# Performance work log

Measured on AMD Instinct MI355X. Metric: run time of the kernel, lower is better.

The kernel has to match this reference:

```python
import jax, jax.numpy as jnp
import numpy as np

B, S, CACHE, HID, NH, NKV, HD, INTER = 2, 1024, 2048, 2048, 8, 1, 256, 16384
EPS = 1e-6
SOFTCAP = 50.0
SCALE = HD ** -0.5  # query_pre_attn_scalar is None -> head_dim**-0.5
NEG = -1e9


def _rms(x, w, eps=EPS):
    # Gemma RMSNorm: fp32 norm, output scaled by (1 + weight)
    x32 = x.astype(jnp.float32)
    n = x32 * jax.lax.rsqrt(jnp.mean(x32 * x32, axis=-1, keepdims=True) + eps)
    return (n * (1.0 + w)).astype(x.dtype)


def _rope(x, cos, sin):
    # half-split complex rotation (Gemma apply_rotary_emb): first half real, second half imag
    d2 = x.shape[-1] // 2
    x1, x2 = x[..., :d2], x[..., d2:]
    c = cos[None, :, None, :]
    s = sin[None, :, None, :]
    return jnp.concatenate([x1 * c - x2 * s, x1 * s + x2 * c], axis=-1).astype(x.dtype)


def setup_inputs() -> dict:
    key = jax.random.key(0)
    ks = jax.random.split(key, 8)
    sc = lambda k, sh, f: jax.random.normal(k, sh, jnp.float32) * f
    inp = {}
    inp["hidden_states"] = sc(ks[0], (B, S, HID), 1.0)
    inv = 1.0 / (10000.0 ** (np.arange(0, HD, 2, dtype=np.float32) / HD))
    t = np.arange(S, dtype=np.float32)[:, None] * inv[None, :]
    inp["cos"] = jnp.asarray(np.cos(t), jnp.float32)
    inp["sin"] = jnp.asarray(np.sin(t), jnp.float32)
    inp["kv_write_indices"] = jnp.arange(S, dtype=jnp.int32)
    inp["k_cache"] = jnp.zeros((B, CACHE, NKV, HD), jnp.float32)
    inp["v_cache"] = jnp.zeros((B, CACHE, NKV, HD), jnp.float32)
    i = jnp.arange(S)[:, None]
    j = jnp.arange(CACHE)[None, :]
    inp["mask"] = jnp.where(j <= i, 0.0, NEG).astype(jnp.float32)[None, None]  # [1,1,S,CACHE]
    inp["w_qkv"] = sc(ks[1], ((NH + 2 * NKV) * HD, HID), 0.02)
    inp["w_o"] = sc(ks[2], (HID, NH * HD), 0.02)
    inp["w_gate"] = sc(ks[3], (INTER, HID), 0.02)
    inp["w_up"] = sc(ks[4], (INTER, HID), 0.02)
    inp["w_down"] = sc(ks[5], (HID, INTER), 0.02)
    inp["ln_in"] = jnp.zeros((HID,), jnp.float32)
    inp["ln_post"] = jnp.zeros((HID,), jnp.float32)
    inp["q_norm"] = jnp.zeros((HD,), jnp.float32)
    inp["k_norm"] = jnp.zeros((HD,), jnp.float32)
    return inp


def reference(hidden_states, cos, sin, kv_write_indices, k_cache, v_cache, mask,
              w_qkv, w_o, w_gate, w_up, w_down, ln_in, ln_post, q_norm, k_norm):
    # ---- attention sub-block ----
    res = hidden_states
    x = _rms(hidden_states, ln_in)
    qkv = x @ w_qkv.T  # [B,S,(NH+2*NKV)*HD]
    xq, xk, xv = jnp.split(qkv, [NH * HD, NH * HD + NKV * HD], axis=-1)
    xq = xq.reshape(B, S, NH, HD)
    xk = xk.reshape(B, S, NKV, HD)
    xv = xv.reshape(B, S, NKV, HD)
    xq = _rms(xq, q_norm)  # QK-norm
    xk = _rms(xk, k_norm)
    xq = _rope(xq, cos, sin)
    xk = _rope(xk, cos, sin)
    # KV-cache write (index_copy_ on dim 1)
    k_cache = k_cache.at[:, kv_write_indices].set(xk)
    v_cache = v_cache.at[:, kv_write_indices].set(xv)
    key = jnp.repeat(k_cache, NH // NKV, axis=2)  # [B,CACHE,NH,HD]
    val = jnp.repeat(v_cache, NH // NKV, axis=2)
    scores = jnp.einsum('bshd,bthd->bhst', xq * SCALE, key)  # [B,NH,S,CACHE]
    scores = jnp.tanh(scores / SOFTCAP) * SOFTCAP            # logit softcapping
    probs = jax.nn.softmax(scores + mask, axis=-1)
    out = jnp.einsum('bhst,bthd->bshd', probs, val).reshape(B, S, NH * HD)
    h = res + out @ w_o.T
    # ---- MLP sub-block ----
    res = h
    x = _rms(h, ln_post)
    gate = jax.nn.gelu(x @ w_gate.T, approximate=True)
    up = x @ w_up.T
    return res + (gate * up) @ w_down.T
```

## Files before the change

### kernel.cpp

```cpp
#include <hip/hip_runtime.h>
#include <hip/hip_bf16.h>

typedef __attribute__((ext_vector_type(8))) short short8;
typedef __attribute__((ext_vector_type(4))) float f32x4;
typedef unsigned short u16;

#define B_N 2
#define S_N 1024
#define HID_N 2048
#define NH_N 8
#define HD_N 256
#define INTER_N 16384

#define GLB(p) ((const __attribute__((address_space(1))) void*)(p))
#define AS3(p) ((__attribute__((address_space(3))) void*)(p))

__device__ inline u16 f2b_rn(float f) {
    union { float f; unsigned int u; } x; x.f = f;
    unsigned int r = x.u + 0x7fffu + ((x.u >> 16) & 1u);
    return (u16)(r >> 16);
}
__device__ inline float b2f(u16 h) {
    union { unsigned int u; float f; } x; x.u = ((unsigned int)h) << 16;
    return x.f;
}
__device__ inline float gelu_tanh(float x) {
    float x3 = x * x * x;
    return 0.5f * x * (1.f + tanhf(0.7978845608028654f * (x + 0.044715f * x3)));
}

__global__ __launch_bounds__(256) void convert_f2b(const float* __restrict__ in,
                                                   u16* __restrict__ out, int n4) {
    int i = blockIdx.x * 256 + threadIdx.x;
    int stride = gridDim.x * 256;
    for (; i < n4; i += stride) {
        float4 v = reinterpret_cast<const float4*>(in)[i];
        u16 o[4] = { f2b_rn(v.x), f2b_rn(v.y), f2b_rn(v.z), f2b_rn(v.w) };
        reinterpret_cast<ulonglong1*>(out)[i] = *reinterpret_cast<ulonglong1*>(o);
    }
}

__global__ __launch_bounds__(256) void rmsnorm_k(const float* __restrict__ x,
                                                 const float* __restrict__ w,
                                                 u16* __restrict__ out) {
    const int row = blockIdx.x;
    const int tid = threadIdx.x;
    const float* xr = x + (size_t)row * HID_N;
    const float4* xr4 = reinterpret_cast<const float4*>(xr);
    float4 a = xr4[tid * 2], b = xr4[tid * 2 + 1];
    float s = a.x*a.x + a.y*a.y + a.z*a.z + a.w*a.w
            + b.x*b.x + b.y*b.y + b.z*b.z + b.w*b.w;
    for (int off = 32; off > 0; off >>= 1) s += __shfl_xor(s, off, 64);
    __shared__ float red[4];
    if ((tid & 63) == 0) red[tid >> 6] = s;
    __syncthreads();
    float tot = red[0] + red[1] + red[2] + red[3];
    float inv = rsqrtf(tot * (1.0f / HID_N) + 1e-6f);
    const float4* w4 = reinterpret_cast<const float4*>(w);
    float4 wa = w4[tid * 2], wb = w4[tid * 2 + 1];
    short8 o;
    o[0] = (short)f2b_rn(a.x * inv * (1.f + wa.x));
    o[1] = (short)f2b_rn(a.y * inv * (1.f + wa.y));
    o[2] = (short)f2b_rn(a.z * inv * (1.f + wa.z));
    o[3] = (short)f2b_rn(a.w * inv * (1.f + wa.w));
    o[4] = (short)f2b_rn(b.x * inv * (1.f + wb.x));
    o[5] = (short)f2b_rn(b.y * inv * (1.f + wb.y));
    o[6] = (short)f2b_rn(b.z * inv * (1.f + wb.z));
    o[7] = (short)f2b_rn(b.w * inv * (1.f + wb.w));
    reinterpret_cast<short8*>(out + (size_t)row * HID_N)[tid] = o;
}

__global__ __launch_bounds__(256) void qkv_post_k(const float* __restrict__ qkv,
                                                  const float* __restrict__ cosb,
                                                  const float* __restrict__ sinb,
                                                  const int* __restrict__ kvw,
                                                  const float* __restrict__ qn,
                                                  const float* __restrict__ kn,
                                                  u16* __restrict__ qb,
                                                  u16* __restrict__ kb,
                                                  u16* __restrict__ vt) {
    const int bs = blockIdx.x;
    const int b = bs >> 10, s = bs & 1023;
    const int tid = threadIdx.x;
    const float* row = qkv + (size_t)bs * 2560;
    __shared__ float buf[256];
    __shared__ float red[4];
    const int sdst = kvw[s];
    const float cv = cosb[s * 128 + (tid & 127)];
    const float sv = sinb[s * 128 + (tid & 127)];
    for (int vi = 0; vi < 9; ++vi) {
        float val = row[vi * 256 + tid];
        float ss = val * val;
        for (int off = 32; off > 0; off >>= 1) ss += __shfl_xor(ss, off, 64);
        __syncthreads();
        if ((tid & 63) == 0) red[tid >> 6] = ss;
        __syncthreads();
        float ms = (red[0] + red[1] + red[2] + red[3]) * (1.f / 256.f) + 1e-6f;
        const float* nw = (vi < 8) ? qn : kn;
        float nrm = val * rsqrtf(ms) * (1.f + nw[tid]);
        buf[tid] = nrm;
        __syncthreads();
        float o;
        if (tid < 128) o = buf[tid] * cv - buf[tid + 128] * sv;
        else           o = buf[tid - 128] * sv + buf[tid] * cv;
        if (vi < 8) {
            qb[(((size_t)(b * 8 + vi)) * 1024 + s) * 256 + tid] = f2b_rn(o * 0.0625f);
        } else {
            kb[((size_t)(b * 1024 + sdst)) * 256 + tid] = f2b_rn(o);
        }
    }
    float vv = row[2304 + tid];
    vt[((size_t)(b * 256 + tid)) * 1024 + sdst] = f2b_rn(vv);
}

__global__ __launch_bounds__(256) void attn_k(const u16* __restrict__ qb,
                                              const u16* __restrict__ kb,
                                              const u16* __restrict__ vt,
                                              float* __restrict__ po,
                                              float* __restrict__ pl) {
    const int qt = blockIdx.x;
    const int h  = blockIdx.y;
    const int c  = blockIdx.z >> 1;
    const int b  = blockIdx.z & 1;
    if (c == 1 && qt < 8) return;
    const int tid = threadIdx.x, lane = tid & 63, wid = tid >> 6;
    const int g = lane >> 4, li = lane & 15;
    const int q0 = qt * 64 + wid * 16;
    const int kv_lo = c * 512;
    __shared__ u16 pbuf[4][16 * 32];

    short8 qf[8];
    const size_t qbase = (((size_t)(b * 8 + h)) * 1024 + q0 + li) * 256;
    #pragma unroll
    for (int kk = 0; kk < 8; ++kk)
        qf[kk] = *reinterpret_cast<const short8*>(qb + qbase + kk * 32 + g * 8);

    f32x4 o[16], o1;
    #pragma unroll
    for (int d = 0; d < 16; ++d) o[d] = f32x4{0.f, 0.f, 0.f, 0.f};
    o1 = f32x4{0.f, 0.f, 0.f, 0.f};
    short8 onesf;
    #pragma unroll
    for (int j = 0; j < 8; ++j) onesf[j] = (short)0x3F80;

    const int nt = (min(kv_lo + 512, q0 + 16) - kv_lo + 31) >> 5;
    const int prd = li * 32 + ((g * 8) ^ (((li >> 2) & 3) * 8));

    for (int t = 0; t < nt; ++t) {
        const int kv0 = kv_lo + t * 32;
        f32x4 sc[2];
        sc[0] = f32x4{0.f, 0.f, 0.f, 0.f};
        sc[1] = f32x4{0.f, 0.f, 0.f, 0.f};
        #pragma unroll
        for (int ch = 0; ch < 2; ++ch) {
            const size_t kbase = ((size_t)(b * 1024 + kv0 + ch * 16 + li)) * 256;
            #pragma unroll
            for (int kk = 0; kk < 8; ++kk) {
                short8 kf = *reinterpret_cast<const short8*>(kb + kbase + kk * 32 + g * 8);
                sc[ch] = __builtin_amdgcn_mfma_f32_16x16x32_bf16(qf[kk], kf, sc[ch], 0, 0, 0);
            }
        }
        #pragma unroll
        for (int reg = 0; reg < 4; ++reg) {
            const int qrow = q0 + g * 4 + reg;
            const int prow = g * 4 + reg;
            const int pswz = ((prow >> 2) & 3) * 8;
            #pragma unroll
            for (int ch = 0; ch < 2; ++ch) {
                const int col = kv0 + ch * 16 + li;
                float s = sc[ch][reg];
                float e = exp2f(s * 0.05770780163555854f);
                float th = 1.f - 2.f * __builtin_amdgcn_rcpf(e + 1.f);
                float pv = exp2f(th * 72.13475204444817f);
                pv = (col <= qrow) ? pv : 0.f;
                pbuf[wid][prow * 32 + ((ch * 16 + li) ^ pswz)] = f2b_rn(pv);
            }
        }
        short8 pf = *reinterpret_cast<const short8*>(&pbuf[wid][prd]);
        o1 = __builtin_amdgcn_mfma_f32_16x16x32_bf16(pf, onesf, o1, 0, 0, 0);
        #pragma unroll
        for (int dth = 0; dth < 2; ++dth) {
            short8 vf[8];
            #pragma unroll
            for (int d8 = 0; d8 < 8; ++d8) {
                const int dt = dth * 8 + d8;
                vf[d8] = *reinterpret_cast<const short8*>(
                    vt + ((size_t)(b * 256 + dt * 16 + li)) * 1024 + kv0 + g * 8);
            }
            #pragma unroll
            for (int d8 = 0; d8 < 8; ++d8)
                o[dth * 8 + d8] = __builtin_amdgcn_mfma_f32_16x16x32_bf16(pf, vf[d8], o[dth * 8 + d8], 0, 0, 0);
        }
    }
    const size_t pbase = ((size_t)((c * 2 + b) * 8 + h)) * 1024;
    #pragma unroll
    for (int reg = 0; reg < 4; ++reg) {
        const int row = q0 + g * 4 + reg;
        #pragma unroll
        for (int dt = 0; dt < 16; ++dt)
            po[(pbase + row) * 256 + dt * 16 + li] = o[dt][reg];
        if (li == 0) pl[pbase + row] = o1[reg];
    }
}

__global__ __launch_bounds__(256) void attn_red_k(const float* __restrict__ po,
                                                  const float* __restrict__ pl,
                                                  u16* __restrict__ out) {
    const int gid = blockIdx.x;
    const int b = gid >> 10, s = gid & 1023;
    const int tid = threadIdx.x;
    const int h = tid >> 5, d0 = (tid & 31) * 8;
    const size_t r0 = ((size_t)(b * 8 + h)) * 1024 + s;
    const size_t r1 = ((size_t)((2 + b) * 8 + h)) * 1024 + s;
    float l = pl[r0];
    float4 a0 = *reinterpret_cast<const float4*>(po + r0 * 256 + d0);
    float4 a1 = *reinterpret_cast<const float4*>(po + r0 * 256 + d0 + 4);
    if (s >= 512) {
        l += pl[r1];
        float4 b0 = *reinterpret_cast<const float4*>(po + r1 * 256 + d0);
        float4 b1 = *reinterpret_cast<const float4*>(po + r1 * 256 + d0 + 4);
        a0.x += b0.x; a0.y += b0.y; a0.z += b0.z; a0.w += b0.w;
        a1.x += b1.x; a1.y += b1.y; a1.z += b1.z; a1.w += b1.w;
    }
    const float inv = 1.f / l;
    u16 r[8] = { f2b_rn(a0.x * inv), f2b_rn(a0.y * inv), f2b_rn(a0.z * inv), f2b_rn(a0.w * inv),
                 f2b_rn(a1.x * inv), f2b_rn(a1.y * inv), f2b_rn(a1.z * inv), f2b_rn(a1.w * inv) };
    *reinterpret_cast<ulonglong2*>(out + ((size_t)gid) * 2048 + h * 256 + d0) =
        *reinterpret_cast<ulonglong2*>(r);
}

template <int EPI>
__global__ __launch_bounds__(256) void gemm_bt(const u16* __restrict__ A,
                                               const u16* __restrict__ W,
                                               const float* __restrict__ res,
                                               float* __restrict__ outf,
                                               int M, int N, int K) {
    __shared__ u16 As[2][128 * 64];
    __shared__ u16 Bs[2][128 * 64];
    const int tid = threadIdx.x, lane = tid & 63, wid = tid >> 6;
    const int g = lane >> 4, li = lane & 15;
    const int wr = wid >> 1, wc = wid & 1;
    const int m0 = blockIdx.x * 128, n0 = blockIdx.y * 128;

    f32x4 acc[4][4];
    #pragma unroll
    for (int m = 0; m < 4; ++m)
        #pragma unroll
        for (int n = 0; n < 4; ++n) acc[m][n] = f32x4{0.f, 0.f, 0.f, 0.f};

    const int lrow = lane >> 3;
    const int lcol = (lane & 7) ^ lrow;
    const u16* ga0 = A + (size_t)(m0 + wid * 32 + lrow) * K + lcol * 8;
    const u16* gb0 = W + (size_t)(n0 + wid * 32 + lrow) * K + lcol * 8;
    const int lbase = wid * 32 * 64;

    auto STAGE = [&](int buf, int k0) {
        #pragma unroll
        for (int i = 0; i < 4; ++i) {
            __builtin_amdgcn_global_load_lds(GLB(ga0 + k0 + (size_t)(i * 8) * K),
                                             AS3(&As[buf][lbase + i * 8 * 64]), 16, 0, 0);
            __builtin_amdgcn_global_load_lds(GLB(gb0 + k0 + (size_t)(i * 8) * K),
                                             AS3(&Bs[buf][lbase + i * 8 * 64]), 16, 0, 0);
        }
    };

    const int NT = K >> 6;
    STAGE(0, 0);
    int cur = 0;
    for (int t = 0; t < NT; ++t) {
        if (t + 1 < NT) {
            STAGE(cur ^ 1, (t + 1) << 6);
            asm volatile("s_waitcnt vmcnt(8)" ::: "memory");
        } else {
            asm volatile("s_waitcnt vmcnt(0)" ::: "memory");
        }
        __builtin_amdgcn_s_barrier();
        __builtin_amdgcn_sched_barrier(0);
        #pragma unroll
        for (int kh = 0; kh < 2; ++kh) {
            short8 af[4], bfr[4];
            #pragma unroll
            for (int m = 0; m < 4; ++m) {
                int rw = wr * 64 + m * 16 + li;
                int slot = (kh * 4 + g) ^ (rw & 7);
                af[m] = *reinterpret_cast<const short8*>(&As[cur][rw * 64 + slot * 8]);
            }
            #pragma unroll
            for (int n = 0; n < 4; ++n) {
                int rw = wc * 64 + n * 16 + li;
                int slot = (kh * 4 + g) ^ (rw & 7);
                bfr[n] = *reinterpret_cast<const short8*>(&Bs[cur][rw * 64 + slot * 8]);
            }
            #pragma unroll
            for (int m = 0; m < 4; ++m)
                #pragma unroll
                for (int n = 0; n < 4; ++n)
                    acc[m][n] = __builtin_amdgcn_mfma_f32_16x16x32_bf16(af[m], bfr[n], acc[m][n], 0, 0, 0);
        }
        __builtin_amdgcn_sched_barrier(0);
        __builtin_amdgcn_s_barrier();
        cur ^= 1;
    }

    #pragma unroll
    for (int m = 0; m < 4; ++m) {
        #pragma unroll
        for (int n = 0; n < 4; ++n) {
            #pragma unroll
            for (int reg = 0; reg < 4; ++reg) {
                int row = m0 + wr * 64 + m * 16 + g * 4 + reg;
                int col = n0 + wc * 64 + n * 16 + li;
                size_t idx = (size_t)row * N + col;
                float v = acc[m][n][reg];
                if (EPI == 0) outf[idx] = v;
                else          outf[idx] = v + res[idx];
            }
        }
    }
}

template <int EPI>
__global__ __launch_bounds__(512, 2) void gemm256(const u16* __restrict__ A,
                                                  const u16* __restrict__ W,
                                                  const u16* __restrict__ gin,
                                                  float* __restrict__ outf,
                                                  u16* __restrict__ outb,
                                                  int M, int N, int K, int kcN) {
    __shared__ u16 As_[2][256 * 64];
    __shared__ u16 Bs_[2][256 * 64];
    const int tid = threadIdx.x, lane = tid & 63, wid = tid >> 6;
    const int g = lane >> 4, li = lane & 15;
    const int wm = wid >> 2, wn = wid & 3;
    const int m0 = blockIdx.x * 256, n0 = blockIdx.y * 256;

    int koff = 0, Keff = K;
    if (EPI == 4) {
        Keff = K / kcN;
        koff = blockIdx.z * Keff;
        outf += (size_t)blockIdx.z * M * N;
    }

    f32x4 acc[8][4];
    #pragma unroll
    for (int m = 0; m < 8; ++m)
        #pragma unroll
        for (int n = 0; n < 4; ++n) acc[m][n] = f32x4{0.f, 0.f, 0.f, 0.f};

    const int trow = tid >> 3;
    const int sgr = (tid & 7) ^ (trow & 7);
    const u16* gaS = A + (size_t)(m0 + trow) * K + koff + sgr * 8;
    const u16* gbS = W + (size_t)(n0 + trow) * K + koff + sgr * 8;
    const int ldst = (wid << 9);

    auto STAGE = [&](int buf, int k0) {
        #pragma unroll
        for (int i = 0; i < 4; ++i)
            __builtin_amdgcn_global_load_lds(GLB(gaS + k0 + (size_t)(i * 64) * K),
                                             AS3(&As_[buf][(i << 12) + ldst]), 16, 0, 0);
        #pragma unroll
        for (int i = 0; i < 4; ++i)
            __builtin_amdgcn_global_load_lds(GLB(gbS + k0 + (size_t)(i * 64) * K),
                                             AS3(&Bs_[buf][(i << 12) + ldst]), 16, 0, 0);
    };

    const int NT = Keff >> 6;
    STAGE(0, 0);
    int cur = 0;
    for (int t = 0; t < NT; ++t) {
        if (t + 1 < NT) {
            STAGE(cur ^ 1, (t + 1) << 6);
            asm volatile("s_waitcnt vmcnt(8)" ::: "memory");
        } else {
            asm volatile("s_waitcnt vmcnt(0)" ::: "memory");
        }
        __builtin_amdgcn_s_barrier();
        __builtin_amdgcn_sched_barrier(0);
        #pragma unroll
        for (int kh = 0; kh < 2; ++kh) {
            short8 af[8], bfr[4];
            #pragma unroll
            for (int m = 0; m < 8; ++m) {
                int rw = wm * 128 + m * 16 + li;
                int slot = (kh * 4 + g) ^ (rw & 7);
                af[m] = *reinterpret_cast<const short8*>(&As_[cur][rw * 64 + slot * 8]);
            }
            #pragma unroll
            for (int n = 0; n < 4; ++n) {
                int rw = wn * 64 + n * 16 + li;
                int slot = (kh * 4 + g) ^ (rw & 7);
                bfr[n] = *reinterpret_cast<const short8*>(&Bs_[cur][rw * 64 + slot * 8]);
            }
            #pragma unroll
            for (int m = 0; m < 8; ++m)
                #pragma unroll
                for (int n = 0; n < 4; ++n)
                    acc[m][n] = __builtin_amdgcn_mfma_f32_16x16x32_bf16(af[m], bfr[n], acc[m][n], 0, 0, 0);
        }
        __builtin_amdgcn_sched_barrier(0);
        __builtin_amdgcn_s_barrier();
        cur ^= 1;
    }

    #pragma unroll
    for (int m = 0; m < 8; ++m) {
        #pragma unroll
        for (int n = 0; n < 4; ++n) {
            #pragma unroll
            for (int reg = 0; reg < 4; ++reg) {
                int row = m0 + wm * 128 + m * 16 + g * 4 + reg;
                int col = n0 + wn * 64 + n * 16 + li;
                size_t idx = (size_t)row * N + col;
                float v = acc[m][n][reg];
                if (EPI == 2)      outb[idx] = f2b_rn(gelu_tanh(v));
                else if (EPI == 3) outb[idx] = f2b_rn(v * b2f(gin[idx]));
                else               outf[idx] = v;
            }
        }
    }
}

__global__ __launch_bounds__(256) void reduce4_k(const float* __restrict__ part,
                                                 const float* __restrict__ res,
                                                 float* __restrict__ out, int n4) {
    int i = blockIdx.x * 256 + threadIdx.x;
    int stride = gridDim.x * 256;
    const size_t ps = (size_t)HID_N * B_N * S_N / 4;
    const float4* p4 = reinterpret_cast<const float4*>(part);
    const float4* r4 = reinterpret_cast<const float4*>(res);
    float4* o4 = reinterpret_cast<float4*>(out);
    for (; i < n4; i += stride) {
        float4 a = p4[i], b = p4[i + ps], c = p4[i + 2 * ps], d = p4[i + 3 * ps];
        float4 r = r4[i];
        float4 o;
        o.x = r.x + a.x + b.x + c.x + d.x;
        o.y = r.y + a.y + b.y + c.y + d.y;
        o.z = r.z + a.z + b.z + c.z + d.z;
        o.w = r.w + a.w + b.w + c.w + d.w;
        o4[i] = o;
    }
}

extern "C" void kernel_launch(void* const* d_in, const int* in_sizes, int n_in,
                              void* d_out, int out_size, void* d_ws, size_t ws_size,
                              hipStream_t stream) {
    (void)in_sizes; (void)n_in; (void)out_size; (void)ws_size;
    const float* hs     = (const float*)d_in[0];
    const float* cosb   = (const float*)d_in[1];
    const float* sinb   = (const float*)d_in[2];
    const int*   kvw    = (const int*)d_in[3];
    const float* wqkv   = (const float*)d_in[7];
    const float* wo     = (const float*)d_in[8];
    const float* wg     = (const float*)d_in[9];
    const float* wu     = (const float*)d_in[10];
    const float* wd     = (const float*)d_in[11];
    const float* ln_in  = (const float*)d_in[12];
    const float* ln_post= (const float*)d_in[13];
    const float* qn     = (const float*)d_in[14];
    const float* kn     = (const float*)d_in[15];
    float* out = (float*)d_out;

    char* p = (char*)d_ws;
    auto alloc = [&](size_t bytes) {
        char* r = p;
        p += (bytes + 255) & ~(size_t)255;
        return r;
    };
    u16* wqkv_b = (u16*)alloc(2560ull * 2048 * 2);
    u16* wo_b   = (u16*)alloc(2048ull * 2048 * 2);
    u16* wg_b   = (u16*)alloc(16384ull * 2048 * 2);
    u16* wu_b   = (u16*)alloc(16384ull * 2048 * 2);
    u16* wd_b   = (u16*)alloc(2048ull * 16384 * 2);
    u16* xn     = (u16*)alloc(2048ull * 2048 * 2);
    float* qkvf = (float*)alloc(2048ull * 2560 * 4);
    u16* qbuf   = (u16*)alloc(2ull * 8 * 1024 * 256 * 2);
    u16* kbuf   = (u16*)alloc(2ull * 1024 * 256 * 2);
    u16* vtbuf  = (u16*)alloc(2ull * 256 * 1024 * 2);
    u16* attn_o = (u16*)alloc(2048ull * 2048 * 2);
    float* hbuf = (float*)alloc(2048ull * 2048 * 4);
    u16* x2     = (u16*)alloc(2048ull * 2048 * 2);
    u16* actb   = (u16*)alloc(2048ull * 16384 * 2);
    float* po   = (float*)alloc(4ull * 8 * 1024 * 256 * 4);
    float* plse = (float*)alloc(4ull * 8 * 1024 * 4);
    float* partials = (float*)d_ws;

    auto conv = [&](const float* src, u16* dst, long n) {
        int n4 = (int)(n / 4);
        long blk = (n4 + 255) / 256;
        if (blk > 4096) blk = 4096;
        convert_f2b<<<dim3((unsigned)blk), dim3(256), 0, stream>>>(src, dst, n4);
    };
    conv(wqkv, wqkv_b, 2560l * 2048);
    conv(wo,   wo_b,   2048l * 2048);
    conv(wg,   wg_b,   16384l * 2048);
    conv(wu,   wu_b,   16384l * 2048);
    conv(wd,   wd_b,   2048l * 16384);

    rmsnorm_k<<<dim3(2048), dim3(256), 0, stream>>>(hs, ln_in, xn);
    gemm_bt<0><<<dim3(16, 20), dim3(256), 0, stream>>>(xn, wqkv_b, nullptr,
                                                       qkvf, 2048, 2560, 2048);
    qkv_post_k<<<dim3(2048), dim3(256), 0, stream>>>(qkvf, cosb, sinb, kvw, qn, kn,
                                                     qbuf, kbuf, vtbuf);
    attn_k<<<dim3(16, 8, 4), dim3(256), 0, stream>>>(qbuf, kbuf, vtbuf, po, plse);
    attn_red_k<<<dim3(2048), dim3(256), 0, stream>>>(po, plse, attn_o);
    gemm_bt<1><<<dim3(16, 16), dim3(256), 0, stream>>>(attn_o, wo_b, hs,
                                                       hbuf, 2048, 2048, 2048);
    rmsnorm_k<<<dim3(2048), dim3(256), 0, stream>>>(hbuf, ln_post, x2);
    gemm256<2><<<dim3(8, 64), dim3(512), 0, stream>>>(x2, wg_b, nullptr,
                                                      nullptr, actb, 2048, 16384, 2048, 1);
    gemm256<3><<<dim3(8, 64), dim3(512), 0, stream>>>(x2, wu_b, actb,
                                                      nullptr, actb, 2048, 16384, 2048, 1);
    gemm256<4><<<dim3(8, 8, 4), dim3(512), 0, stream>>>(actb, wd_b, nullptr,
                                                        partials, nullptr, 2048, 2048, 16384, 4);
    reduce4_k<<<dim3(2048), dim3(256), 0, stream>>>(partials, hbuf, out, 1048576);
}
```

Baseline: 890.5 us.

## Pipeline 256x256 GEMM in quadrant phases with interleaved LDS staging and priority hints

Restructures the main 256x256 GEMM loop so each K-tile is computed as four quadrant sub-products. Global-to-LDS loads of the next tiles are spread across those phases, with setprio raised around MFMA bursts so memory traffic overlaps compute instead of bunching at the tile boundary. The warp-to-tile mapping changes to split M and N into halves. The GELU epilogue also replaces tanhf with an exp2 and reciprocal form. The cost is more barriers, more complex waitcnt bookkeeping, and slight numeric differences in GELU.

```diff
diff --git a/kernel.cpp b/kernel.cpp
--- a/kernel.cpp
+++ b/kernel.cpp
@@ -24,9 +24,11 @@
     union { unsigned int u; float f; } x; x.u = ((unsigned int)h) << 16;
     return x.f;
 }
-__device__ inline float gelu_tanh(float x) {
-    float x3 = x * x * x;
-    return 0.5f * x * (1.f + tanhf(0.7978845608028654f * (x + 0.044715f * x3)));
+__device__ inline float gelu_fast(float v) {
+    float z = 0.7978845608028654f * (v + 0.044715f * v * v * v);
+    float e = exp2f(z * 2.8853900817779268f);
+    float th = 1.f - 2.f * __builtin_amdgcn_rcpf(e + 1.f);
+    return 0.5f * v * (1.f + th);
 }
 
 __global__ __launch_bounds__(256) void convert_f2b(const float* __restrict__ in,
@@ -326,8 +328,8 @@
                                                   float* __restrict__ outf,
                                                   u16* __restrict__ outb,
                                                   int M, int N, int K, int kcN) {
-    __shared__ u16 As_[2][256 * 64];
-    __shared__ u16 Bs_[2][256 * 64];
+    __shared__ u16 Als[2][256 * 64];
+    __shared__ u16 Bls[2][256 * 64];
     const int tid = threadIdx.x, lane = tid & 63, wid = tid >> 6;
     const int g = lane >> 4, li = lane & 15;
     const int wm = wid >> 2, wn = wid & 3;
@@ -346,72 +348,129 @@
         #pragma unroll
         for (int n = 0; n < 4; ++n) acc[m][n] = f32x4{0.f, 0.f, 0.f, 0.f};
 
-    const int trow = tid >> 3;
-    const int sgr = (tid & 7) ^ (trow & 7);
-    const u16* gaS = A + (size_t)(m0 + trow) * K + koff + sgr * 8;
-    const u16* gbS = W + (size_t)(n0 + trow) * K + koff + sgr * 8;
-    const int ldst = (wid << 9);
-
-    auto STAGE = [&](int buf, int k0) {
-        #pragma unroll
-        for (int i = 0; i < 4; ++i)
-            __builtin_amdgcn_global_load_lds(GLB(gaS + k0 + (size_t)(i * 64) * K),
-                                             AS3(&As_[buf][(i << 12) + ldst]), 16, 0, 0);
-        #pragma unroll
-        for (int i = 0; i < 4; ++i)
-            __builtin_amdgcn_global_load_lds(GLB(gbS + k0 + (size_t)(i * 64) * K),
-                                             AS3(&Bs_[buf][(i << 12) + ldst]), 16, 0, 0);
+    const int srcg = ((tid & 7) ^ ((tid >> 3) & 7)) * 8;
+    const u16* Asrc = A + (size_t)(m0 + (tid >> 3)) * K + koff + srcg;
+    const u16* Bsrc = W + (size_t)(n0 + (tid >> 3)) * K + koff + srcg;
+    const int dstb = wid * 512;
+
+    auto STAGE_A = [&](int bf, int h, int kt) {
+        const int k0 = kt << 6;
+        #pragma unroll
+        for (int i = 0; i < 2; ++i)
+            __builtin_amdgcn_global_load_lds(GLB(Asrc + (size_t)(h * 128 + i * 64) * K + k0),
+                                             AS3(&Als[bf][h * 8192 + i * 4096 + dstb]), 16, 0, 0);
+    };
+    auto STAGE_B = [&](int bf, int h, int kt) {
+        const int k0 = kt << 6;
+        #pragma unroll
+        for (int i = 0; i < 2; ++i)
+            __builtin_amdgcn_global_load_lds(GLB(Bsrc + (size_t)(h * 128 + i * 64) * K + k0),
+                                             AS3(&Bls[bf][h * 8192 + i * 4096 + dstb]), 16, 0, 0);
+    };
+    auto LDA = [&](short8* d, int mh, int cb) {
+        #pragma unroll
+        for (int m = 0; m < 4; ++m) {
+            const int rw = mh * 128 + wm * 64 + m * 16 + li;
+            #pragma unroll
+            for (int kh = 0; kh < 2; ++kh) {
+                const int slot = (kh * 4 + g) ^ (rw & 7);
+                d[m * 2 + kh] = *reinterpret_cast<const short8*>(&Als[cb][rw * 64 + slot * 8]);
+            }
+        }
+    };
+    auto LDB = [&](short8* d, int nh, int cb) {
+        #pragma unroll
+        for (int n = 0; n < 2; ++n) {
+            const int rw = nh * 128 + wn * 32 + n * 16 + li;
+            #pragma unroll
+            for (int kh = 0; kh < 2; ++kh) {
+                const int slot = (kh * 4 + g) ^ (rw & 7);
+                d[n * 2 + kh] = *reinterpret_cast<const short8*>(&Bls[cb][rw * 64 + slot * 8]);
+            }
+        }
+    };
+
+    short8 af[8], bq0[4], bq1[4];
+    auto MQ = [&](int mh, int nh, short8* bb) {
+        #pragma unroll
+        for (int m = 0; m < 4; ++m)
+            #pragma unroll
+            for (int n = 0; n < 2; ++n)
+                #pragma unroll
+                for (int kh = 0; kh < 2; ++kh)
+                    acc[mh * 4 + m][nh * 2 + n] = __builtin_amdgcn_mfma_f32_16x16x32_bf16(
+                        af[m * 2 + kh], bb[n * 2 + kh], acc[mh * 4 + m][nh * 2 + n], 0, 0, 0);
     };
 
     const int NT = Keff >> 6;
-    STAGE(0, 0);
+    STAGE_A(0, 0, 0); STAGE_B(0, 0, 0); STAGE_B(0, 1, 0); STAGE_A(0, 1, 0);
+    {
+        const int t1 = (1 < NT) ? 1 : NT - 1;
+        STAGE_A(1, 0, t1); STAGE_B(1, 0, t1); STAGE_B(1, 1, t1);
+    }
+    asm volatile("s_waitcnt vmcnt(6)" ::: "memory");
+    __builtin_amdgcn_s_barrier();
+    __builtin_amdgcn_sched_barrier(0);
+
     int cur = 0;
     for (int t = 0; t < NT; ++t) {
-        if (t + 1 < NT) {
-            STAGE(cur ^ 1, (t + 1) << 6);
-            asm volatile("s_waitcnt vmcnt(8)" ::: "memory");
-        } else {
-            asm volatile("s_waitcnt vmcnt(0)" ::: "memory");
-        }
-        __builtin_amdgcn_s_barrier();
-        __builtin_amdgcn_sched_barrier(0);
-        #pragma unroll
-        for (int kh = 0; kh < 2; ++kh) {
-            short8 af[8], bfr[4];
-            #pragma unroll
-            for (int m = 0; m < 8; ++m) {
-                int rw = wm * 128 + m * 16 + li;
-                int slot = (kh * 4 + g) ^ (rw & 7);
-                af[m] = *reinterpret_cast<const short8*>(&As_[cur][rw * 64 + slot * 8]);
-            }
-            #pragma unroll
-            for (int n = 0; n < 4; ++n) {
-                int rw = wn * 64 + n * 16 + li;
-                int slot = (kh * 4 + g) ^ (rw & 7);
-                bfr[n] = *reinterpret_cast<const short8*>(&Bs_[cur][rw * 64 + slot * 8]);
-            }
-            #pragma unroll
-            for (int m = 0; m < 8; ++m)
-                #pragma unroll
-                for (int n = 0; n < 4; ++n)
-                    acc[m][n] = __builtin_amdgcn_mfma_f32_16x16x32_bf16(af[m], bfr[n], acc[m][n], 0, 0, 0);
-        }
-        __builtin_amdgcn_sched_barrier(0);
-        __builtin_amdgcn_s_barrier();
+        const int tp1 = (t + 1 < NT) ? t + 1 : NT - 1;
+        const int tp2 = (t + 2 < NT) ? t + 2 : NT - 1;
+        LDA(af, 0, cur); LDB(bq0, 0, cur);
+        STAGE_A(cur ^ 1, 1, tp1);
+        __builtin_amdgcn_s_barrier();
+        asm volatile("s_waitcnt lgkmcnt(0)" ::: "memory");
+        __builtin_amdgcn_sched_barrier(0);
+        __builtin_amdgcn_s_setprio(1);
+        MQ(0, 0, bq0);
+        __builtin_amdgcn_s_setprio(0);
+        __builtin_amdgcn_s_barrier();
+        __builtin_amdgcn_sched_barrier(0);
+        LDB(bq1, 1, cur);
+        STAGE_A(cur, 0, tp2);
+        __builtin_amdgcn_s_barrier();
+        asm volatile("s_waitcnt lgkmcnt(0)" ::: "memory");
+        __builtin_amdgcn_sched_barrier(0);
+        __builtin_amdgcn_s_setprio(1);
+        MQ(0, 1, bq1);
+        __builtin_amdgcn_s_setprio(0);
+        __builtin_amdgcn_s_barrier();
+        __builtin_amdgcn_sched_barrier(0);
+        LDA(af, 1, cur);
+        STAGE_B(cur, 0, tp2);
+        __builtin_amdgcn_s_barrier();
+        asm volatile("s_waitcnt lgkmcnt(0)" ::: "memory");
+        __builtin_amdgcn_sched_barrier(0);
+        __builtin_amdgcn_s_setprio(1);
+        MQ(1, 1, bq1);
+        __builtin_amdgcn_s_setprio(0);
+        __builtin_amdgcn_s_barrier();
+        __builtin_amdgcn_sched_barrier(0);
+        STAGE_B(cur, 1, tp2);
+        __builtin_amdgcn_s_barrier();
+        __builtin_amdgcn_sched_barrier(0);
+        __builtin_amdgcn_s_setprio(1);
+        MQ(1, 0, bq0);
+        __builtin_amdgcn_s_setprio(0);
+        asm volatile("s_waitcnt vmcnt(6)" ::: "memory");
+        __builtin_amdgcn_s_barrier();
+        __builtin_amdgcn_sched_barrier(0);
         cur ^= 1;
     }
 
     #pragma unroll
-    for (int m = 0; m < 8; ++m) {
-        #pragma unroll
-        for (int n = 0; n < 4; ++n) {
+    for (int mg = 0; mg < 8; ++mg) {
+        const int mh = mg >> 2, m = mg & 3;
+        #pragma unroll
+        for (int ng = 0; ng < 4; ++ng) {
+            const int nh = ng >> 1, n = ng & 1;
             #pragma unroll
             for (int reg = 0; reg < 4; ++reg) {
-                int row = m0 + wm * 128 + m * 16 + g * 4 + reg;
-                int col = n0 + wn * 64 + n * 16 + li;
+                const int row = m0 + mh * 128 + wm * 64 + m * 16 + g * 4 + reg;
+                const int col = n0 + nh * 128 + wn * 32 + n * 16 + li;
                 size_t idx = (size_t)row * N + col;
-                float v = acc[m][n][reg];
-                if (EPI == 2)      outb[idx] = f2b_rn(gelu_tanh(v));
+                float v = acc[mg][ng][reg];
+                if (EPI == 2)      outb[idx] = f2b_rn(gelu_fast(v));
                 else if (EPI == 3) outb[idx] = f2b_rn(v * b2f(gin[idx]));
                 else               outf[idx] = v;
             }
```

Measured after the change: 908.4 us. 1.02x slower.
